# Kernel tuning notes

Hardware: AMD Instinct MI355X
Metric: run time of the kernel (lower is better)

Reference implementation:

```python
import jax, jax.numpy as jnp
import numpy as np

B, H, N, D = 4, 8, 2048, 64  # d_model=512, n_heads=8 -> d_head=64
MASK_PROB = 0.1
SCALE = D ** -0.5


def setup_inputs() -> dict:
    key = jax.random.key(0)
    kq, kk, kv, km = jax.random.split(key, 4)
    q = jax.random.normal(kq, (B, H, N, D), dtype=jnp.float32)
    k = jax.random.normal(kk, (B, H, N, D), dtype=jnp.float32)
    v = jax.random.normal(kv, (B, H, N, D), dtype=jnp.float32)
    # torch.bernoulli(full(..., prob)): 1 with prob=mask_prob -> dropped
    mask = jax.random.bernoulli(km, MASK_PROB, (B, H, N, N))
    return {"q": q, "k": k, "v": v, "mask": mask}


def reference(q, k, v, mask):
    # [B,H,N,N] scores: QK^T * scale -> tanh -> zero where mask is True
    scores = jnp.tanh(jnp.einsum("bhnd,bhmd->bhnm", q, k) * SCALE)
    scores = scores * (~mask).astype(scores.dtype)
    return jnp.einsum("bhnm,bhmd->bhnd", scores, v)
```

## Files before the change

kernel.cpp:

```cpp
#include <hip/hip_runtime.h>

namespace {

constexpr int N = 2048;
constexpr int D = 64;
constexpr float SCALE = 0.125f;
constexpr int LK = 72;
constexpr int LV = 68;
constexpr int NT = N / 64;
constexpr int BH = 32;
constexpr size_t NKV    = (size_t)BH * N * D;
constexpr size_t NMASK  = (size_t)BH * N * N;
constexpr size_t NWORDS = NMASK / 64;

typedef __attribute__((ext_vector_type(8))) short bf16x8;
typedef __attribute__((ext_vector_type(4))) short short4v;
typedef __attribute__((ext_vector_type(2))) short short2v;
typedef __attribute__((ext_vector_type(4))) float f32x4;

__device__ inline short f2bf(float x) {
  union { float f; unsigned u; } a; a.f = x;
  unsigned r = a.u + 0x7fffu + ((a.u >> 16) & 1u);
  return (short)(r >> 16);
}

#if __has_builtin(__builtin_amdgcn_cvt_pk_bf16_f32)
typedef __attribute__((ext_vector_type(2))) __bf16 bfv2;
__device__ inline short2v pk_bf(float lo, float hi) {
  bfv2 t = __builtin_amdgcn_cvt_pk_bf16_f32(lo, hi);
  return __builtin_bit_cast(short2v, t);
}
#else
__device__ inline short2v pk_bf(float lo, float hi) {
  short2v r; r[0] = f2bf(lo); r[1] = f2bf(hi); return r;
}
#endif

__device__ inline short4v pk4(float4 f) {
  short2v a = pk_bf(f.x, f.y), b = pk_bf(f.z, f.w);
  short4v r; r[0] = a[0]; r[1] = a[1]; r[2] = b[0]; r[3] = b[1];
  return r;
}

__device__ inline float fast_tanh(float x) {
  float e = __builtin_amdgcn_exp2f(x * 2.885390081777927f);
  return 1.0f - 2.0f * __builtin_amdgcn_rcpf(e + 1.0f);
}

}

__global__ __launch_bounds__(256) void cvt_kv_bf16(
    const float* __restrict__ K, const float* __restrict__ V,
    short* __restrict__ KB, short* __restrict__ VB)
{
  const int n4 = (int)(NKV / 4);
  const int stride = gridDim.x * blockDim.x;
  for (int j = blockIdx.x * blockDim.x + threadIdx.x; j < n4; j += stride) {
    ((short4v*)KB)[j] = pk4(((const float4*)K)[j]);
    ((short4v*)VB)[j] = pk4(((const float4*)V)[j]);
  }
}

__global__ __launch_bounds__(256) void mask_pack(
    const int* __restrict__ M, unsigned long long* __restrict__ W)
{
  const int lane = threadIdx.x & 63;
  const size_t g = (size_t)blockIdx.x * 4 + (threadIdx.x >> 6);
  const size_t steps = NWORDS / 8192;
  const int* p = M + (g * steps) * 64 + lane;
  unsigned long long* w = W + g * steps;
  for (size_t s = 0; s < steps; s += 8) {
    int v[8];
#pragma unroll
    for (int j = 0; j < 8; ++j)
      v[j] = __builtin_nontemporal_load(p + (s + j) * 64);
    unsigned long long b[8];
#pragma unroll
    for (int j = 0; j < 8; ++j) b[j] = __ballot(v[j] != 0);
    if (lane == 0) {
#pragma unroll
      for (int j = 0; j < 8; ++j) w[s + j] = b[j];
    }
  }
}

__global__ __launch_bounds__(256, 4) void attn_tanh_kernel(
    const float* __restrict__ Q, const short* __restrict__ KB,
    const short* __restrict__ VB, const unsigned long long* __restrict__ MW,
    float* __restrict__ O)
{
  __shared__ __align__(16) short k_s[64 * LK];
  __shared__ __align__(16) short s_s[64 * LK];
  __shared__ __align__(16) short vt_s[64 * LV];

  const int tid  = threadIdx.x;
  const int wave = tid >> 6;
  const int lane = tid & 63;
  const int l15  = lane & 15;
  const int quad = lane >> 4;

  const int bh = blockIdx.x & 31;
  const int q0 = (blockIdx.x >> 5) * 64;

  const float* qp = Q + (size_t)bh * N * D;
  float* op = O + (size_t)bh * N * D;
  const short* kpb = KB + (size_t)bh * N * D;
  const short* vpb = VB + (size_t)bh * N * D;
  const short* vbase = vpb + (size_t)(wave * 16) * D + lane;
  const unsigned long long* mwb =
      MW + ((size_t)bh * N + q0 + wave * 16 + l15) * NT;

  bf16x8 qf[2];
  {
    const float* qrow = qp + (size_t)(q0 + wave * 16 + l15) * D + quad * 8;
#pragma unroll
    for (int ks = 0; ks < 2; ++ks) {
      float4 f0 = *(const float4*)(qrow + ks * 32);
      float4 f1 = *(const float4*)(qrow + ks * 32 + 4);
      short4v lo = pk4(f0), hi = pk4(f1);
      bf16x8 t;
      t[0]=lo[0]; t[1]=lo[1]; t[2]=lo[2]; t[3]=lo[3];
      t[4]=hi[0]; t[5]=hi[1]; t[6]=hi[2]; t[7]=hi[3];
      qf[ks] = t;
    }
  }

  const int krow = tid >> 3;
  const int kcol = (tid & 7) * 8;
  bf16x8 kreg2[2];
  short  vregb[16];
  unsigned long long mreg;

  auto issue_loads = [&](int kt1) {
    const short* kt_ = kpb + (size_t)kt1 * 64 * D;
#pragma unroll
    for (int i = 0; i < 2; ++i)
      kreg2[i] = *(const bf16x8*)(kt_ + (size_t)(krow + i * 32) * D + kcol);
    const short* vt_ = vbase + (size_t)kt1 * 64 * D;
#pragma unroll
    for (int i = 0; i < 16; ++i)
      vregb[i] = vt_[(size_t)i * D];
    mreg = mwb[kt1];
  };

  auto write_kv = [&]() {
#pragma unroll
    for (int i = 0; i < 2; ++i)
      *(bf16x8*)(&k_s[(krow + i * 32) * LK + kcol]) = kreg2[i];
#pragma unroll
    for (int c = 0; c < 4; ++c) {
      short4v vv;
      vv[0] = vregb[4*c+0]; vv[1] = vregb[4*c+1];
      vv[2] = vregb[4*c+2]; vv[3] = vregb[4*c+3];
      *(short4v*)(&vt_s[lane * LV + wave * 16 + 4 * c]) = vv;
    }
  };

  issue_loads(0);

  f32x4 o_acc[4];
#pragma unroll
  for (int i = 0; i < 4; ++i) o_acc[i] = (f32x4){0.f, 0.f, 0.f, 0.f};

  for (int kt = 0; kt < NT; ++kt) {
    __syncthreads();
    write_kv();
    __syncthreads();

    const unsigned long long mcur = mreg;

#pragma unroll
    for (int ct = 0; ct < 4; ++ct) {
      f32x4 acc = {0.f, 0.f, 0.f, 0.f};
#pragma unroll
      for (int ksi = 0; ksi < 2; ++ksi) {
        bf16x8 a = *(const bf16x8*)(&k_s[(ct * 16 + l15) * LK + ksi * 32 + quad * 8]);
        acc = __builtin_amdgcn_mfma_f32_16x16x32_bf16(a, qf[ksi], acc, 0, 0, 0);
      }
      const unsigned mn = (unsigned)(mcur >> (ct * 16 + quad * 4)) & 0xFu;
      float s0 = (mn & 1u) ? 0.f : fast_tanh(acc[0] * SCALE);
      float s1 = (mn & 2u) ? 0.f : fast_tanh(acc[1] * SCALE);
      float s2 = (mn & 4u) ? 0.f : fast_tanh(acc[2] * SCALE);
      float s3 = (mn & 8u) ? 0.f : fast_tanh(acc[3] * SCALE);
      short2v p0 = pk_bf(s0, s1), p1 = pk_bf(s2, s3);
      short4v sv; sv[0]=p0[0]; sv[1]=p0[1]; sv[2]=p1[0]; sv[3]=p1[1];
      *(short4v*)(&s_s[(wave * 16 + l15) * LK + ct * 16 + quad * 4]) = sv;
    }

    if (kt + 1 < NT) issue_loads(kt + 1);

#pragma unroll
    for (int ksi = 0; ksi < 2; ++ksi) {
      bf16x8 a = *(const bf16x8*)(&s_s[(wave * 16 + l15) * LK + ksi * 32 + quad * 8]);
#pragma unroll
      for (int nt = 0; nt < 4; ++nt) {
        const short* vb = &vt_s[(nt * 16 + l15) * LV + ksi * 32 + quad * 8];
        short4v lo = *(const short4v*)(vb);
        short4v hi = *(const short4v*)(vb + 4);
        bf16x8 b = __builtin_shufflevector(lo, hi, 0, 1, 2, 3, 4, 5, 6, 7);
        o_acc[nt] = __builtin_amdgcn_mfma_f32_16x16x32_bf16(a, b, o_acc[nt], 0, 0, 0);
      }
    }
  }

#pragma unroll
  for (int nt = 0; nt < 4; ++nt) {
#pragma unroll
    for (int r = 0; r < 4; ++r) {
      op[(q0 + wave * 16 + quad * 4 + r) * D + nt * 16 + l15] = o_acc[nt][r];
    }
  }
}

extern "C" void kernel_launch(void* const* d_in, const int* in_sizes, int n_in,
                              void* d_out, int out_size, void* d_ws, size_t ws_size,
                              hipStream_t stream) {
  const float* q = (const float*)d_in[0];
  const float* k = (const float*)d_in[1];
  const float* v = (const float*)d_in[2];
  const int*   m = (const int*)d_in[3];
  float* out = (float*)d_out;

  short* kb = (short*)d_ws;
  short* vb = kb + NKV;
  unsigned long long* mw = (unsigned long long*)(vb + NKV);

  cvt_kv_bf16<<<dim3(2048), dim3(256), 0, stream>>>(k, v, kb, vb);
  mask_pack<<<dim3(2048), dim3(256), 0, stream>>>(m, mw);
  attn_tanh_kernel<<<dim3(1024), dim3(256), 0, stream>>>(q, kb, vb, mw, out);
}
```

Baseline: 787.6 us.

## Use 32x32x16 MFMA tiles with pre-transposed V in global memory

Replaces the 16x16x32 MFMA tiling with 32x32x16 MFMAs, splitting the 64x64 score tile and the output tile into four 32x32 quadrants, one per wave. V is now transposed to bf16 by a separate preprocessing kernel, so the main loop loads V with wide vector loads instead of sixteen scalar strided loads and a register transpose. Next-tile prefetch now starts before the QK matmul. The cost is an extra __syncthreads per tile, because each wave's S quadrant is read by other waves. The launch_bounds occupancy hint is dropped and one more preprocessing kernel is launched.

New measurement: 784.3 us. No clear change (-0.4%).

```diff
diff --git a/kernel.cpp b/kernel.cpp
--- a/kernel.cpp
+++ b/kernel.cpp
@@ -5,18 +5,17 @@
 constexpr int N = 2048;
 constexpr int D = 64;
 constexpr float SCALE = 0.125f;
-constexpr int LK = 72;
-constexpr int LV = 68;
+constexpr int LS = 72;
 constexpr int NT = N / 64;
 constexpr int BH = 32;
 constexpr size_t NKV    = (size_t)BH * N * D;
 constexpr size_t NMASK  = (size_t)BH * N * N;
 constexpr size_t NWORDS = NMASK / 64;
 
-typedef __attribute__((ext_vector_type(8))) short bf16x8;
-typedef __attribute__((ext_vector_type(4))) short short4v;
-typedef __attribute__((ext_vector_type(2))) short short2v;
-typedef __attribute__((ext_vector_type(4))) float f32x4;
+typedef __attribute__((ext_vector_type(8)))  short bf16x8;
+typedef __attribute__((ext_vector_type(4)))  short short4v;
+typedef __attribute__((ext_vector_type(2)))  short short2v;
+typedef __attribute__((ext_vector_type(16))) float f32x16;
 
 __device__ inline short f2bf(float x) {
   union { float f; unsigned u; } a; a.f = x;
@@ -49,16 +48,40 @@
 
 }
 
-__global__ __launch_bounds__(256) void cvt_kv_bf16(
-    const float* __restrict__ K, const float* __restrict__ V,
-    short* __restrict__ KB, short* __restrict__ VB)
+__global__ __launch_bounds__(256) void cvt_k_bf16(
+    const float* __restrict__ K, short* __restrict__ KB)
 {
   const int n4 = (int)(NKV / 4);
   const int stride = gridDim.x * blockDim.x;
-  for (int j = blockIdx.x * blockDim.x + threadIdx.x; j < n4; j += stride) {
+  for (int j = blockIdx.x * blockDim.x + threadIdx.x; j < n4; j += stride)
     ((short4v*)KB)[j] = pk4(((const float4*)K)[j]);
-    ((short4v*)VB)[j] = pk4(((const float4*)V)[j]);
-  }
+}
+
+__global__ __launch_bounds__(256) void transpose_v_bf16(
+    const float* __restrict__ V, short* __restrict__ VT)
+{
+  __shared__ short tl[64 * 68];
+  const int tid = threadIdx.x;
+  const int bh  = blockIdx.x >> 5;
+  const int kp0 = (blockIdx.x & 31) * 64;
+  const float* vp = V + ((size_t)bh * N + kp0) * D;
+#pragma unroll
+  for (int i = 0; i < 4; ++i) {
+    int idx = i * 256 + tid;
+    int row = idx >> 4, c4 = (idx & 15) << 2;
+    *(short4v*)(&tl[row * 68 + c4]) = pk4(*(const float4*)(vp + (size_t)row * D + c4));
+  }
+  __syncthreads();
+  const int d  = tid >> 2;
+  const int ch = (tid & 3) * 16;
+  short* out = VT + (size_t)bh * D * N + (size_t)d * N + kp0 + ch;
+  bf16x8 o0, o1;
+#pragma unroll
+  for (int j = 0; j < 8; ++j) o0[j] = tl[(ch + j) * 68 + d];
+#pragma unroll
+  for (int j = 0; j < 8; ++j) o1[j] = tl[(ch + 8 + j) * 68 + d];
+  *(bf16x8*)(out)     = o0;
+  *(bf16x8*)(out + 8) = o1;
 }
 
 __global__ __launch_bounds__(256) void mask_pack(
@@ -84,83 +107,78 @@
   }
 }
 
-__global__ __launch_bounds__(256, 4) void attn_tanh_kernel(
+__global__ __launch_bounds__(256) void attn_tanh_kernel(
     const float* __restrict__ Q, const short* __restrict__ KB,
-    const short* __restrict__ VB, const unsigned long long* __restrict__ MW,
+    const short* __restrict__ VT, const unsigned long long* __restrict__ MW,
     float* __restrict__ O)
 {
-  __shared__ __align__(16) short k_s[64 * LK];
-  __shared__ __align__(16) short s_s[64 * LK];
-  __shared__ __align__(16) short vt_s[64 * LV];
+  __shared__ __align__(16) short k_s[64 * LS];
+  __shared__ __align__(16) short vt_s[64 * LS];
+  __shared__ __align__(16) short s_s[64 * LS];
 
   const int tid  = threadIdx.x;
   const int wave = tid >> 6;
   const int lane = tid & 63;
-  const int l15  = lane & 15;
-  const int quad = lane >> 4;
+  const int l31  = lane & 31;
+  const int half = lane >> 5;
+
+  const int sa = wave & 1, sb = wave >> 1;
+  const int qh = wave & 1, dh = wave >> 1;
 
   const int bh = blockIdx.x & 31;
   const int q0 = (blockIdx.x >> 5) * 64;
 
-  const float* qp = Q + (size_t)bh * N * D;
+  const short* kpb = KB + (size_t)bh * N * D;
+  const short* vtb = VT + (size_t)bh * D * N;
   float* op = O + (size_t)bh * N * D;
-  const short* kpb = KB + (size_t)bh * N * D;
-  const short* vpb = VB + (size_t)bh * N * D;
-  const short* vbase = vpb + (size_t)(wave * 16) * D + lane;
-  const unsigned long long* mwb =
-      MW + ((size_t)bh * N + q0 + wave * 16 + l15) * NT;
-
-  bf16x8 qf[2];
+
+  bf16x8 qf[4];
   {
-    const float* qrow = qp + (size_t)(q0 + wave * 16 + l15) * D + quad * 8;
-#pragma unroll
-    for (int ks = 0; ks < 2; ++ks) {
-      float4 f0 = *(const float4*)(qrow + ks * 32);
-      float4 f1 = *(const float4*)(qrow + ks * 32 + 4);
+    const float* qrow = Q + ((size_t)bh * N + q0 + 32 * sb + l31) * D;
+#pragma unroll
+    for (int st = 0; st < 4; ++st) {
+      int d0 = 16 * st + 8 * half;
+      float4 f0 = *(const float4*)(qrow + d0);
+      float4 f1 = *(const float4*)(qrow + d0 + 4);
       short4v lo = pk4(f0), hi = pk4(f1);
       bf16x8 t;
       t[0]=lo[0]; t[1]=lo[1]; t[2]=lo[2]; t[3]=lo[3];
       t[4]=hi[0]; t[5]=hi[1]; t[6]=hi[2]; t[7]=hi[3];
-      qf[ks] = t;
-    }
-  }
+      qf[st] = t;
+    }
+  }
+
+  const unsigned long long* mwb =
+      MW + ((size_t)bh * N + q0 + 32 * sb + l31) * NT;
 
   const int krow = tid >> 3;
   const int kcol = (tid & 7) * 8;
-  bf16x8 kreg2[2];
-  short  vregb[16];
+  bf16x8 kreg[2], vreg[2];
   unsigned long long mreg;
 
   auto issue_loads = [&](int kt1) {
-    const short* kt_ = kpb + (size_t)kt1 * 64 * D;
-#pragma unroll
-    for (int i = 0; i < 2; ++i)
-      kreg2[i] = *(const bf16x8*)(kt_ + (size_t)(krow + i * 32) * D + kcol);
-    const short* vt_ = vbase + (size_t)kt1 * 64 * D;
-#pragma unroll
-    for (int i = 0; i < 16; ++i)
-      vregb[i] = vt_[(size_t)i * D];
+    const short* kp_ = kpb + (size_t)kt1 * 64 * D;
+#pragma unroll
+    for (int i = 0; i < 2; ++i)
+      kreg[i] = *(const bf16x8*)(kp_ + (size_t)(krow + 32 * i) * D + kcol);
+#pragma unroll
+    for (int i = 0; i < 2; ++i)
+      vreg[i] = *(const bf16x8*)(vtb + (size_t)(krow + 32 * i) * N + kt1 * 64 + kcol);
     mreg = mwb[kt1];
   };
 
   auto write_kv = [&]() {
 #pragma unroll
     for (int i = 0; i < 2; ++i)
-      *(bf16x8*)(&k_s[(krow + i * 32) * LK + kcol]) = kreg2[i];
-#pragma unroll
-    for (int c = 0; c < 4; ++c) {
-      short4v vv;
-      vv[0] = vregb[4*c+0]; vv[1] = vregb[4*c+1];
-      vv[2] = vregb[4*c+2]; vv[3] = vregb[4*c+3];
-      *(short4v*)(&vt_s[lane * LV + wave * 16 + 4 * c]) = vv;
-    }
+      *(bf16x8*)(&k_s[(krow + 32 * i) * LS + kcol]) = kreg[i];
+#pragma unroll
+    for (int i = 0; i < 2; ++i)
+      *(bf16x8*)(&vt_s[(krow + 32 * i) * LS + kcol]) = vreg[i];
   };
 
   issue_loads(0);
 
-  f32x4 o_acc[4];
-#pragma unroll
-  for (int i = 0; i < 4; ++i) o_acc[i] = (f32x4){0.f, 0.f, 0.f, 0.f};
+  f32x16 o_acc = {};
 
   for (int kt = 0; kt < NT; ++kt) {
     __syncthreads();
@@ -168,47 +186,40 @@
     __syncthreads();
 
     const unsigned long long mcur = mreg;
-
-#pragma unroll
-    for (int ct = 0; ct < 4; ++ct) {
-      f32x4 acc = {0.f, 0.f, 0.f, 0.f};
-#pragma unroll
-      for (int ksi = 0; ksi < 2; ++ksi) {
-        bf16x8 a = *(const bf16x8*)(&k_s[(ct * 16 + l15) * LK + ksi * 32 + quad * 8]);
-        acc = __builtin_amdgcn_mfma_f32_16x16x32_bf16(a, qf[ksi], acc, 0, 0, 0);
-      }
-      const unsigned mn = (unsigned)(mcur >> (ct * 16 + quad * 4)) & 0xFu;
-      float s0 = (mn & 1u) ? 0.f : fast_tanh(acc[0] * SCALE);
-      float s1 = (mn & 2u) ? 0.f : fast_tanh(acc[1] * SCALE);
-      float s2 = (mn & 4u) ? 0.f : fast_tanh(acc[2] * SCALE);
-      float s3 = (mn & 8u) ? 0.f : fast_tanh(acc[3] * SCALE);
+    if (kt + 1 < NT) issue_loads(kt + 1);
+
+    f32x16 sacc = {};
+#pragma unroll
+    for (int st = 0; st < 4; ++st) {
+      bf16x8 a = *(const bf16x8*)(&k_s[(32 * sa + l31) * LS + 16 * st + 8 * half]);
+      sacc = __builtin_amdgcn_mfma_f32_32x32x16_bf16(a, qf[st], sacc, 0, 0, 0);
+    }
+#pragma unroll
+    for (int g = 0; g < 4; ++g) {
+      const int kpb_loc = 32 * sa + 8 * g + 4 * half;
+      const unsigned bits = (unsigned)(mcur >> kpb_loc) & 0xFu;
+      float s0 = (bits & 1u) ? 0.f : fast_tanh(sacc[4 * g + 0] * SCALE);
+      float s1 = (bits & 2u) ? 0.f : fast_tanh(sacc[4 * g + 1] * SCALE);
+      float s2 = (bits & 4u) ? 0.f : fast_tanh(sacc[4 * g + 2] * SCALE);
+      float s3 = (bits & 8u) ? 0.f : fast_tanh(sacc[4 * g + 3] * SCALE);
       short2v p0 = pk_bf(s0, s1), p1 = pk_bf(s2, s3);
       short4v sv; sv[0]=p0[0]; sv[1]=p0[1]; sv[2]=p1[0]; sv[3]=p1[1];
-      *(short4v*)(&s_s[(wave * 16 + l15) * LK + ct * 16 + quad * 4]) = sv;
-    }
-
-    if (kt + 1 < NT) issue_loads(kt + 1);
-
-#pragma unroll
-    for (int ksi = 0; ksi < 2; ++ksi) {
-      bf16x8 a = *(const bf16x8*)(&s_s[(wave * 16 + l15) * LK + ksi * 32 + quad * 8]);
-#pragma unroll
-      for (int nt = 0; nt < 4; ++nt) {
-        const short* vb = &vt_s[(nt * 16 + l15) * LV + ksi * 32 + quad * 8];
-        short4v lo = *(const short4v*)(vb);
-        short4v hi = *(const short4v*)(vb + 4);
-        bf16x8 b = __builtin_shufflevector(lo, hi, 0, 1, 2, 3, 4, 5, 6, 7);
-        o_acc[nt] = __builtin_amdgcn_mfma_f32_16x16x32_bf16(a, b, o_acc[nt], 0, 0, 0);
-      }
-    }
-  }
-
-#pragma unroll
-  for (int nt = 0; nt < 4; ++nt) {
-#pragma unroll
-    for (int r = 0; r < 4; ++r) {
-      op[(q0 + wave * 16 + quad * 4 + r) * D + nt * 16 + l15] = o_acc[nt][r];
-    }
+      *(short4v*)(&s_s[(32 * sb + l31) * LS + kpb_loc]) = sv;
+    }
+    __syncthreads();
+
+#pragma unroll
+    for (int st = 0; st < 4; ++st) {
+      bf16x8 a = *(const bf16x8*)(&s_s[(32 * qh + l31) * LS + 16 * st + 8 * half]);
+      bf16x8 b = *(const bf16x8*)(&vt_s[(32 * dh + l31) * LS + 16 * st + 8 * half]);
+      o_acc = __builtin_amdgcn_mfma_f32_32x32x16_bf16(a, b, o_acc, 0, 0, 0);
+    }
+  }
+
+#pragma unroll
+  for (int reg = 0; reg < 16; ++reg) {
+    const int qr = q0 + 32 * qh + (reg & 3) + 8 * (reg >> 2) + 4 * half;
+    op[(size_t)qr * D + 32 * dh + l31] = o_acc[reg];
   }
 }
 
@@ -222,10 +233,11 @@
   float* out = (float*)d_out;
 
   short* kb = (short*)d_ws;
-  short* vb = kb + NKV;
-  unsigned long long* mw = (unsigned long long*)(vb + NKV);
-
-  cvt_kv_bf16<<<dim3(2048), dim3(256), 0, stream>>>(k, v, kb, vb);
+  short* vt = kb + NKV;
+  unsigned long long* mw = (unsigned long long*)(vt + NKV);
+
+  cvt_k_bf16<<<dim3(1024), dim3(256), 0, stream>>>(k, kb);
+  transpose_v_bf16<<<dim3(1024), dim3(256), 0, stream>>>(v, vt);
   mask_pack<<<dim3(2048), dim3(256), 0, stream>>>(m, mw);
-  attn_tanh_kernel<<<dim3(1024), dim3(256), 0, stream>>>(q, kb, vb, mw, out);
-}
+  attn_tanh_kernel<<<dim3(1024), dim3(256), 0, stream>>>(q, kb, vt, mw, out);
+}
```
